# Kernel tuning notes

Hardware: AMD Instinct MI355X
Metric: run time of the kernel (lower is better)

## Reference

```python
import jax, jax.numpy as jnp
import numpy as np

ALPHA = 0.0005
TAU = 0.2


def setup_inputs() -> dict:
    key = jax.random.key(0)
    k1, k2, k3 = jax.random.split(key, 3)
    output = jax.random.normal(k1, (8192, 1000), dtype=jnp.float32)
    target = jax.random.normal(k2, (8192, 1000), dtype=jnp.float32)
    conv_w = jax.random.normal(k3, (256, 256, 128, 3), dtype=jnp.float32)
    return {"output": output, "target": target, "conv_w": conv_w}


def reference(output, target, conv_w):
    # base loss (nn.MSELoss with default 'mean' reduction)
    loss = jnp.mean((output - target) ** 2)

    # Diversity regularizer: pairwise cosine similarity between slices
    # conv_w[:, :, i, :] along dim 2 ('filters' = size(2) in the original).
    F = conv_w.shape[2]
    # V: [F, D] with D = out_ch * in_ch * kw
    V = jnp.transpose(conv_w, (2, 0, 1, 3)).reshape(F, -1)
    norms = jnp.linalg.norm(V, axis=1)                      # [F]
    G = (V @ V.T) / (norms[:, None] * norms[None, :])       # [F, F] cosine Gram

    # keep entries with tau < sim <= 1 and i != j
    offdiag = ~jnp.eye(F, dtype=bool)
    mask = (G > TAU) & (G <= 1.0) & offdiag
    reg = jnp.sum(jnp.where(mask, G, jnp.zeros((), dtype=G.dtype)))

    return loss + ALPHA * reg
```

## Files before the change

### kernel.cpp

```cpp
#include <hip/hip_runtime.h>
#include <hip/hip_bf16.h>


typedef __attribute__((ext_vector_type(8))) short bf16x8;
typedef __attribute__((ext_vector_type(4))) float f32x4;

#define ALPHA 0.0005f
#define TAU 0.2f

#define FDIM 128
#define TSTRIDE 52
#define GRAM_NBLK 512
#define CHUNK_F4 3072
#define GRAM_ELEMS 16384
#define NPAIRQ 8192
#define MSE_N4 2048000
#define MSE_NBLK 2048

__device__ __forceinline__ unsigned int pack_bf2(float lo, float hi) {
    union { float f; unsigned int u; } a, b;
    a.f = lo; b.f = hi;
    unsigned int al = (a.u + 0x7fffu + ((a.u >> 16) & 1u)) >> 16;
    unsigned int bh = (b.u + 0x7fffu + ((b.u >> 16) & 1u)) & 0xffff0000u;
    return (al & 0xffffu) | bh;
}

__global__ void __launch_bounds__(256) mse_kernel(
        const float* __restrict__ o, const float* __restrict__ t,
        float* __restrict__ mse_part) {
    __shared__ float red[4];
    const int tid = threadIdx.x;
    const float4* o4 = reinterpret_cast<const float4*>(o);
    const float4* t4 = reinterpret_cast<const float4*>(t);
    float s = 0.f;
    for (int i = blockIdx.x * 256 + tid; i < MSE_N4; i += MSE_NBLK * 256) {
        float4 a = o4[i], b = t4[i];
        float dx = a.x - b.x, dy = a.y - b.y, dz = a.z - b.z, dw = a.w - b.w;
        s += dx * dx + dy * dy + dz * dz + dw * dw;
    }
    for (int off = 32; off; off >>= 1) s += __shfl_down(s, off);
    if ((tid & 63) == 0) red[tid >> 6] = s;
    __syncthreads();
    if (tid == 0) mse_part[blockIdx.x] = red[0] + red[1] + red[2] + red[3];
}

__global__ void __launch_bounds__(512, 6) gram_kernel(
        const float* __restrict__ conv, unsigned int* __restrict__ pp) {
    __shared__ unsigned int tile[FDIM * TSTRIDE];
    const int tid = threadIdx.x;
    const int lane = tid & 63;
    const int wave = tid >> 6;
    const int sp = tid >> 5;
    const int q = tid & 31;
    const int colr = lane & 15;
    const int hi8 = (lane >> 4) * 8;
    const unsigned short* tileu = reinterpret_cast<const unsigned short*>(tile);

    f32x4 acc0[8];
#pragma unroll
    for (int cc = 0; cc < 8; ++cc) acc0[cc] = (f32x4)0.f;

    const f32x4* src4 = reinterpret_cast<const f32x4*>(conv);
    const size_t cb = (size_t)blockIdx.x * (4 * CHUNK_F4) + sp * 192 + q;

    for (int c = 0; c < 4; ++c) {
        __syncthreads();
        f32x4 V0[3], V1[3];
#pragma unroll
        for (int it = 0; it < 3; ++it) {
            V0[it] = src4[cb + c * CHUNK_F4 + 32 * it];
            V1[it] = src4[cb + c * CHUNK_F4 + 96 + 32 * it];
        }
#pragma unroll
        for (int it = 0; it < 3; ++it)
#pragma unroll
            for (int u = 0; u < 4; ++u) {
                const int idx = (q + 32 * it) * 4 + u;
                const int f = idx / 3;
                const int k = idx - 3 * f;
                tile[f * TSTRIDE + k * 16 + sp] = pack_bf2(V0[it][u], V1[it][u]);
            }
        __syncthreads();
#pragma unroll
        for (int ks = 0; ks < 3; ++ks) {
            const int koff = ks * 32 + hi8;
            bf16x8 a0 = *reinterpret_cast<const bf16x8*>(
                &tileu[(wave * 16 + colr) * (TSTRIDE * 2) + koff]);
#pragma unroll
            for (int cc = 0; cc < 8; ++cc) {
                bf16x8 b = *reinterpret_cast<const bf16x8*>(
                    &tileu[(cc * 16 + colr) * (TSTRIDE * 2) + koff]);
                acc0[cc] = __builtin_amdgcn_mfma_f32_16x16x32_bf16(a0, b, acc0[cc], 0, 0, 0);
            }
        }
    }

    unsigned int* myp = pp + (size_t)blockIdx.x * NPAIRQ;
    const int rsub = (lane >> 4) << 2;
#pragma unroll
    for (int cc = 0; cc < 4; ++cc) {
        const int clo = cc * 16 + colr;
#pragma unroll
        for (int j = 0; j < 4; ++j) {
            const int row = wave * 16 + rsub + j;
            myp[row * 64 + clo] = pack_bf2(acc0[cc][j], acc0[cc + 4][j]);
        }
    }
}

__global__ void __launch_bounds__(256) reduce_kernel(
        const unsigned int* __restrict__ pp, float* __restrict__ gram) {
    __shared__ float red[16][16][2];
    const int tid = threadIdx.x;
    const int u = tid & 15;
    const int s = tid >> 4;
    const int qq = blockIdx.x * 16 + u;
    float lo = 0.f, hi = 0.f;
#pragma unroll 8
    for (int b = s * 32; b < s * 32 + 32; ++b) {
        const unsigned int v = pp[(size_t)b * NPAIRQ + qq];
        lo += __uint_as_float(v << 16);
        hi += __uint_as_float(v & 0xffff0000u);
    }
    red[s][u][0] = lo; red[s][u][1] = hi;
    __syncthreads();
    if (tid < 32) {
        const int u2 = tid >> 1, h = tid & 1;
        float x = 0.f;
#pragma unroll
        for (int s2 = 0; s2 < 16; ++s2) x += red[s2][u2][h];
        gram[(blockIdx.x * 16 + u2) * 2 + h] = x;
    }
}

__global__ void __launch_bounds__(256) finalize_kernel(
        const float* __restrict__ gram, const float* __restrict__ mse_part,
        float* __restrict__ out) {
    __shared__ float rn[FDIM];
    __shared__ float redS[4], redM[4];
    const int tid = threadIdx.x;
    if (tid < FDIM) {
        const int r = tid;
        rn[r] = rsqrtf(gram[(r * 64 + (r & 63)) * 2 + (r >> 6)]);
    }
    __syncthreads();
    float s = 0.f;
    for (int i = tid; i < GRAM_ELEMS; i += 256) {
        const int h = i & 1;
        const int qq = i >> 1;
        const int row = qq >> 6;
        const int col = (qq & 63) | (h << 6);
        const float gv = gram[i] * rn[row] * rn[col];
        if (row != col && gv > TAU && gv <= 1.0f) s += gv;
    }
    float m = 0.f;
#pragma unroll 8
    for (int j = 0; j < 8; ++j) m += mse_part[tid * 8 + j];
    for (int off = 32; off; off >>= 1) {
        s += __shfl_down(s, off);
        m += __shfl_down(m, off);
    }
    if ((tid & 63) == 0) { redS[tid >> 6] = s; redM[tid >> 6] = m; }
    __syncthreads();
    if (tid == 0)
        out[0] = (redM[0] + redM[1] + redM[2] + redM[3]) * (1.0f / 8192000.0f) +
                 ALPHA * (redS[0] + redS[1] + redS[2] + redS[3]);
}

extern "C" void kernel_launch(void* const* d_in, const int* in_sizes, int n_in,
                              void* d_out, int out_size, void* d_ws, size_t ws_size,
                              hipStream_t stream) {
    const float* output = (const float*)d_in[0];
    const float* target = (const float*)d_in[1];
    const float* conv   = (const float*)d_in[2];
    float* out = (float*)d_out;

    float* wsf       = (float*)d_ws;
    float* mse_part  = wsf;
    float* gram      = wsf + MSE_NBLK;
    unsigned int* pp = (unsigned int*)(wsf + MSE_NBLK + GRAM_ELEMS);
    (void)ws_size;

    gram_kernel<<<GRAM_NBLK, 512, 0, stream>>>(conv, pp);
    mse_kernel<<<MSE_NBLK, 256, 0, stream>>>(output, target, mse_part);
    reduce_kernel<<<NPAIRQ / 16, 256, 0, stream>>>(pp, gram);
    finalize_kernel<<<1, 256, 0, stream>>>(gram, mse_part, out);
}
```

Baseline: 66.44 us.

## Restructure Gram kernel to 1024 smaller blocks with padded-K tiles and 2x register tiling

The Gram kernel now runs 1024 blocks of 256 threads instead of 512 blocks of 512 threads. Each thread loads contiguous float3 triplets and writes packed bf16 rows with zero-padded K directly into a smaller shared tile, which replaces the div-by-3 scatter. Each wave computes two 16-row A fragments against shared B fragments (acc0/acc1), so B fragment loads are reused. The partial-product layout changes, so the reduce kernel now sums 1024 partials per pair and finalize remaps its indices. Padding K from 3 to 4 per pair wastes a quarter of the MFMA work, and doubling the partials doubles reduce traffic.

Result: faster. 64.92 us (-2.3%).

```diff
diff --git a/kernel.cpp b/kernel.cpp
--- a/kernel.cpp
+++ b/kernel.cpp
@@ -9,11 +9,11 @@
 #define TAU 0.2f
 
 #define FDIM 128
-#define TSTRIDE 52
-#define GRAM_NBLK 512
-#define CHUNK_F4 3072
+#define TSD 20
+#define NGRAM 1024
+#define BLK_FLOATS 24576
+#define NPAIRQ 8192
 #define GRAM_ELEMS 16384
-#define NPAIRQ 8192
 #define MSE_N4 2048000
 #define MSE_NBLK 2048
 
@@ -23,6 +23,11 @@
     unsigned int al = (a.u + 0x7fffu + ((a.u >> 16) & 1u)) >> 16;
     unsigned int bh = (b.u + 0x7fffu + ((b.u >> 16) & 1u)) & 0xffff0000u;
     return (al & 0xffffu) | bh;
+}
+__device__ __forceinline__ unsigned int pack_bf1(float lo) {
+    union { float f; unsigned int u; } a;
+    a.f = lo;
+    return (a.u + 0x7fffu + ((a.u >> 16) & 1u)) >> 16;
 }
 
 __global__ void __launch_bounds__(256) mse_kernel(
@@ -44,66 +49,62 @@
     if (tid == 0) mse_part[blockIdx.x] = red[0] + red[1] + red[2] + red[3];
 }
 
-__global__ void __launch_bounds__(512, 6) gram_kernel(
+__global__ void __launch_bounds__(256, 4) gram_kernel(
         const float* __restrict__ conv, unsigned int* __restrict__ pp) {
-    __shared__ unsigned int tile[FDIM * TSTRIDE];
+    __shared__ unsigned int tile[FDIM * TSD];
     const int tid = threadIdx.x;
     const int lane = tid & 63;
     const int wave = tid >> 6;
-    const int sp = tid >> 5;
-    const int q = tid & 31;
+    const int row = tid & 127;
+    const int pr = tid >> 7;
     const int colr = lane & 15;
     const int hi8 = (lane >> 4) * 8;
     const unsigned short* tileu = reinterpret_cast<const unsigned short*>(tile);
 
-    f32x4 acc0[8];
+    f32x4 acc0[8], acc1[8];
 #pragma unroll
-    for (int cc = 0; cc < 8; ++cc) acc0[cc] = (f32x4)0.f;
+    for (int cc = 0; cc < 8; ++cc) { acc0[cc] = (f32x4)0.f; acc1[cc] = (f32x4)0.f; }
 
-    const f32x4* src4 = reinterpret_cast<const f32x4*>(conv);
-    const size_t cb = (size_t)blockIdx.x * (4 * CHUNK_F4) + sp * 192 + q;
+    const float* bp = conv + (size_t)blockIdx.x * BLK_FLOATS + row * 3;
 
-    for (int c = 0; c < 4; ++c) {
+    for (int c = 0; c < 8; ++c) {
         __syncthreads();
-        f32x4 V0[3], V1[3];
+        const float* cp = bp + c * 3072;
 #pragma unroll
-        for (int it = 0; it < 3; ++it) {
-            V0[it] = src4[cb + c * CHUNK_F4 + 32 * it];
-            V1[it] = src4[cb + c * CHUNK_F4 + 96 + 32 * it];
+        for (int z = 0; z < 2; ++z) {
+            const int p2 = pr + 2 * z;
+            const float3 A = *reinterpret_cast<const float3*>(cp + (2 * p2) * 384);
+            const float3 B = *reinterpret_cast<const float3*>(cp + (2 * p2) * 384 + 384);
+            uint4 w;
+            w.x = pack_bf2(A.x, A.y);
+            w.y = pack_bf1(A.z);
+            w.z = pack_bf2(B.x, B.y);
+            w.w = pack_bf1(B.z);
+            *reinterpret_cast<uint4*>(&tile[row * TSD + p2 * 4]) = w;
         }
+        __syncthreads();
+        bf16x8 a0 = *reinterpret_cast<const bf16x8*>(
+            &tileu[(wave * 32 + colr) * (TSD * 2) + hi8]);
+        bf16x8 a1 = *reinterpret_cast<const bf16x8*>(
+            &tileu[(wave * 32 + 16 + colr) * (TSD * 2) + hi8]);
 #pragma unroll
-        for (int it = 0; it < 3; ++it)
-#pragma unroll
-            for (int u = 0; u < 4; ++u) {
-                const int idx = (q + 32 * it) * 4 + u;
-                const int f = idx / 3;
-                const int k = idx - 3 * f;
-                tile[f * TSTRIDE + k * 16 + sp] = pack_bf2(V0[it][u], V1[it][u]);
-            }
-        __syncthreads();
-#pragma unroll
-        for (int ks = 0; ks < 3; ++ks) {
-            const int koff = ks * 32 + hi8;
-            bf16x8 a0 = *reinterpret_cast<const bf16x8*>(
-                &tileu[(wave * 16 + colr) * (TSTRIDE * 2) + koff]);
-#pragma unroll
-            for (int cc = 0; cc < 8; ++cc) {
-                bf16x8 b = *reinterpret_cast<const bf16x8*>(
-                    &tileu[(cc * 16 + colr) * (TSTRIDE * 2) + koff]);
-                acc0[cc] = __builtin_amdgcn_mfma_f32_16x16x32_bf16(a0, b, acc0[cc], 0, 0, 0);
-            }
+        for (int cc = 0; cc < 8; ++cc) {
+            bf16x8 b = *reinterpret_cast<const bf16x8*>(
+                &tileu[(cc * 16 + colr) * (TSD * 2) + hi8]);
+            acc0[cc] = __builtin_amdgcn_mfma_f32_16x16x32_bf16(a0, b, acc0[cc], 0, 0, 0);
+            acc1[cc] = __builtin_amdgcn_mfma_f32_16x16x32_bf16(a1, b, acc1[cc], 0, 0, 0);
         }
     }
 
     unsigned int* myp = pp + (size_t)blockIdx.x * NPAIRQ;
     const int rsub = (lane >> 4) << 2;
 #pragma unroll
-    for (int cc = 0; cc < 4; ++cc) {
-        const int clo = cc * 16 + colr;
+    for (int cc = 0; cc < 8; ++cc) {
+        const int col = cc * 16 + colr;
 #pragma unroll
         for (int j = 0; j < 4; ++j) {
-            const int row = wave * 16 + rsub + j;
-            myp[row * 64 + clo] = pack_bf2(acc0[cc][j], acc0[cc + 4][j]);
+            const int pr2 = wave * 16 + rsub + j;
+            myp[pr2 * FDIM + col] = pack_bf2(acc0[cc][j], acc1[cc][j]);
         }
     }
 }
@@ -117,7 +118,7 @@
     const int qq = blockIdx.x * 16 + u;
     float lo = 0.f, hi = 0.f;
 #pragma unroll 8
-    for (int b = s * 32; b < s * 32 + 32; ++b) {
+    for (int b = s * 64; b < s * 64 + 64; ++b) {
         const unsigned int v = pp[(size_t)b * NPAIRQ + qq];
         lo += __uint_as_float(v << 16);
         hi += __uint_as_float(v & 0xffff0000u);
@@ -140,16 +141,19 @@
     __shared__ float redS[4], redM[4];
     const int tid = threadIdx.x;
     if (tid < FDIM) {
-        const int r = tid;
-        rn[r] = rsqrtf(gram[(r * 64 + (r & 63)) * 2 + (r >> 6)]);
+        const int row = tid;
+        const int pr2 = (row >> 5) * 16 + (row & 15);
+        const int h = (row >> 4) & 1;
+        rn[row] = rsqrtf(gram[(pr2 * FDIM + row) * 2 + h]);
     }
     __syncthreads();
     float s = 0.f;
     for (int i = tid; i < GRAM_ELEMS; i += 256) {
         const int h = i & 1;
         const int qq = i >> 1;
-        const int row = qq >> 6;
-        const int col = (qq & 63) | (h << 6);
+        const int col = qq & 127;
+        const int pr2 = qq >> 7;
+        const int row = (pr2 >> 4) * 32 + (pr2 & 15) + (h << 4);
         const float gv = gram[i] * rn[row] * rn[col];
         if (row != col && gv > TAU && gv <= 1.0f) s += gv;
     }
@@ -181,7 +185,7 @@
     unsigned int* pp = (unsigned int*)(wsf + MSE_NBLK + GRAM_ELEMS);
     (void)ws_size;
 
-    gram_kernel<<<GRAM_NBLK, 512, 0, stream>>>(conv, pp);
+    gram_kernel<<<NGRAM, 256, 0, stream>>>(conv, pp);
     mse_kernel<<<MSE_NBLK, 256, 0, stream>>>(output, target, mse_part);
     reduce_kernel<<<NPAIRQ / 16, 256, 0, stream>>>(pp, gram);
     finalize_kernel<<<1, 256, 0, stream>>>(gram, mse_part, out);
```
